# Kernel optimization log

Measured on AMD Instinct MI355X. Metric: run time of the kernel, lower is better.

Reference implementation:

```python
import jax, jax.numpy as jnp
import numpy as np

EPS = 1e-6


def setup_inputs() -> dict:
    key = jax.random.key(0)
    k1, k2 = jax.random.split(key)
    S, B, H, F = 4096, 8, 1024, 1024
    x = jax.random.normal(k1, (S, B, H), dtype=jnp.float32)
    scale = jnp.ones((H,), dtype=jnp.float32)
    ln_bias = jnp.zeros((H,), dtype=jnp.float32)
    # variance_scaling(1.0, 'fan_in', 'truncated_normal') ~ normal with std 1/sqrt(fan_in)
    kernel = jax.random.normal(k2, (H, F), dtype=jnp.float32) * (1.0 / np.sqrt(H))
    return {"x": x, "scale": scale, "ln_bias": ln_bias, "kernel": kernel}


def reference(x, scale, ln_bias, kernel):
    # LayerNorm over last (hidden) axis; zero_centered_gamma=False:
    #   y = (x - mean) / sqrt(var + eps) * gamma + beta
    mu = jnp.mean(x, axis=-1, keepdims=True)
    var = jnp.mean(jnp.square(x - mu), axis=-1, keepdims=True)
    ln_out = (x - mu) * jax.lax.rsqrt(var + EPS) * scale + ln_bias
    # DenseGeneral: contract hidden axis with kernel (H, F); use_bias=False, no depth scaling
    out = jnp.einsum("sbh,hf->sbf", ln_out, kernel)
    # return_layernorm_output=True -> (out, ln_out)
    return (out, ln_out)
```

## Files before the change

### kernel.cpp

```cpp
#include <hip/hip_runtime.h>
#include <stdint.h>

typedef unsigned short u16;

#define S_ 4096
#define B_ 8
#define H_ 1024
#define F_ 1024
#define M_ (S_ * B_)
#define N_ F_
#define K_ H_

#define BM 256
#define BN 256
#define BK 64
#define NT (K_ / BK)

typedef short short8 __attribute__((ext_vector_type(8)));
typedef float floatx4 __attribute__((ext_vector_type(4)));

__device__ __forceinline__ u16 f2bf(float f) {
    union { float f; uint32_t u; } c;
    c.f = f;
    uint32_t u = c.u;
    uint32_t r = (u + 0x7fffu + ((u >> 16) & 1u)) >> 16;
    return (u16)r;
}

__device__ __forceinline__ void async_load16(const void* gptr, void* lptr) {
    __builtin_amdgcn_global_load_lds(
        (const __attribute__((address_space(1))) uint32_t*)gptr,
        (__attribute__((address_space(3))) uint32_t*)lptr,
        16 , 0 , 0 );
}

__global__ __launch_bounds__(256) void transpose_cast_kernel(
    const float* __restrict__ w, u16* __restrict__ bt)
{
    __shared__ float tile[32][33];
    const int tx = threadIdx.x;
    const int ty = threadIdx.y;
    const int n0 = blockIdx.x * 32;
    const int k0 = blockIdx.y * 32;
#pragma unroll
    for (int j = 0; j < 4; ++j)
        tile[ty + j * 8][tx] = w[(size_t)(k0 + ty + j * 8) * N_ + n0 + tx];
    __syncthreads();
#pragma unroll
    for (int j = 0; j < 4; ++j)
        bt[(size_t)(n0 + ty + j * 8) * K_ + k0 + tx] =
            f2bf(tile[tx][ty + j * 8]);
}

#define LN_BLOCKS 2048
__global__ __launch_bounds__(256) void ln_kernel(
    const float* __restrict__ x, const float* __restrict__ scale,
    const float* __restrict__ bias, float* __restrict__ ln_out,
    u16* __restrict__ ln_bf16)
{
    const int lane = threadIdx.x & 63;
    const int wid  = (blockIdx.x << 2) | (threadIdx.x >> 6);
    const int nwaves = LN_BLOCKS * 4;

    float4 sc[4], bi[4];
#pragma unroll
    for (int j = 0; j < 4; ++j) {
        sc[j] = reinterpret_cast<const float4*>(scale)[j * 64 + lane];
        bi[j] = reinterpret_cast<const float4*>(bias)[j * 64 + lane];
    }

    for (int row = wid; row < M_; row += nwaves) {
        const float4* xr = reinterpret_cast<const float4*>(x + (size_t)row * H_);
        float4 v[4];
        float s = 0.f, sq = 0.f;
#pragma unroll
        for (int j = 0; j < 4; ++j) {
            v[j] = xr[j * 64 + lane];
            s  += v[j].x + v[j].y + v[j].z + v[j].w;
            sq += v[j].x * v[j].x + v[j].y * v[j].y +
                  v[j].z * v[j].z + v[j].w * v[j].w;
        }
#pragma unroll
        for (int off = 32; off >= 1; off >>= 1) {
            s  += __shfl_xor(s, off, 64);
            sq += __shfl_xor(sq, off, 64);
        }
        const float mu   = s * (1.0f / H_);
        const float var  = sq * (1.0f / H_) - mu * mu;
        const float rstd = rsqrtf(var + 1e-6f);

        float4* yr = reinterpret_cast<float4*>(ln_out + (size_t)row * H_);
        ushort4* hr = reinterpret_cast<ushort4*>(ln_bf16 + (size_t)row * H_);
#pragma unroll
        for (int j = 0; j < 4; ++j) {
            float4 y;
            y.x = (v[j].x - mu) * rstd * sc[j].x + bi[j].x;
            y.y = (v[j].y - mu) * rstd * sc[j].y + bi[j].y;
            y.z = (v[j].z - mu) * rstd * sc[j].z + bi[j].z;
            y.w = (v[j].w - mu) * rstd * sc[j].w + bi[j].w;
            yr[j * 64 + lane] = y;
            ushort4 h;
            h.x = f2bf(y.x); h.y = f2bf(y.y); h.z = f2bf(y.z); h.w = f2bf(y.w);
            hr[j * 64 + lane] = h;
        }
    }
}

__global__ __launch_bounds__(512, 2) void gemm_bt_kernel(
    const u16* __restrict__ A, const u16* __restrict__ Bt,
    float* __restrict__ C)
{
    __shared__ __align__(16) u16 As[2][BM * BK];
    __shared__ __align__(16) u16 Bs[2][BN * BK];

    const int tid  = threadIdx.x;
    const int wid  = tid >> 6;
    const int lane = tid & 63;
    const int wm   = wid >> 2;
    const int wn   = wid & 3;

    const int bid  = blockIdx.x;
    const int bx   = (bid >> 3) & 3;
    const int by   = ((bid >> 5) << 3) | (bid & 7);
    const int row0 = by * BM;
    const int col0 = bx * BN;

    floatx4 acc[8][4];
#pragma unroll
    for (int i = 0; i < 8; ++i)
#pragma unroll
        for (int j = 0; j < 4; ++j) acc[i][j] = (floatx4)0.0f;

    const int srow   = (wid << 3) | (lane >> 3);
    const int schunk = (lane & 7) ^ (srow & 7);
    const u16* Ag = A  + (size_t)(row0 + srow) * K_ + schunk * 8;
    const u16* Bg = Bt + (size_t)(col0 + srow) * K_ + schunk * 8;

#define STAGE(buf, kt) do {                                                   \
    const size_t koff_ = (size_t)(kt) * BK;                                   \
    _Pragma("unroll")                                                         \
    for (int i_ = 0; i_ < 4; ++i_) {                                          \
        async_load16(Ag + (size_t)(i_ * 64) * K_ + koff_,                     \
                     (char*)As[buf] + (size_t)(i_ * 64 + (wid << 3)) * 128);  \
        async_load16(Bg + (size_t)(i_ * 64) * K_ + koff_,                     \
                     (char*)Bs[buf] + (size_t)(i_ * 64 + (wid << 3)) * 128);  \
    }                                                                         \
} while (0)

    STAGE(0, 0);
    STAGE(1, 1);
    asm volatile("s_waitcnt vmcnt(8)" ::: "memory");
    __builtin_amdgcn_s_barrier();

    int cur = 0;
    for (int t = 0; t < NT; ++t) {
        short8 bfrag[4][2];
#pragma unroll
        for (int nt = 0; nt < 4; ++nt)
#pragma unroll
            for (int ks = 0; ks < 2; ++ks) {
                const int r  = (wn << 6) | (nt << 4) | (lane & 15);
                const int q  = (ks << 2) | (lane >> 4);
                const int cc = q ^ (r & 7);
                bfrag[nt][ks] = *reinterpret_cast<const short8*>(
                    (const char*)Bs[cur] + (size_t)r * 128 + cc * 16);
            }
#pragma unroll
        for (int mp = 0; mp < 4; ++mp) {
            short8 afrag[2][2];
#pragma unroll
            for (int mi = 0; mi < 2; ++mi)
#pragma unroll
                for (int ks = 0; ks < 2; ++ks) {
                    const int mt = mp * 2 + mi;
                    const int r  = (wm << 7) | (mt << 4) | (lane & 15);
                    const int q  = (ks << 2) | (lane >> 4);
                    const int cc = q ^ (r & 7);
                    afrag[mi][ks] = *reinterpret_cast<const short8*>(
                        (const char*)As[cur] + (size_t)r * 128 + cc * 16);
                }
            __builtin_amdgcn_s_setprio(1);
#pragma unroll
            for (int mi = 0; mi < 2; ++mi)
#pragma unroll
                for (int nt = 0; nt < 4; ++nt)
#pragma unroll
                    for (int ks = 0; ks < 2; ++ks)
                        acc[mp * 2 + mi][nt] =
                            __builtin_amdgcn_mfma_f32_16x16x32_bf16(
                                afrag[mi][ks], bfrag[nt][ks],
                                acc[mp * 2 + mi][nt], 0, 0, 0);
            __builtin_amdgcn_s_setprio(0);
        }

        if (t == NT - 1) break;
        asm volatile("s_waitcnt vmcnt(0) lgkmcnt(0)" ::: "memory");
        __builtin_amdgcn_s_barrier();
        if (t + 2 < NT) STAGE(cur, t + 2);
        cur ^= 1;
    }
#undef STAGE

#pragma unroll
    for (int mt = 0; mt < 8; ++mt) {
#pragma unroll
        for (int nt = 0; nt < 4; ++nt) {
            const int r0 = row0 + (wm << 7) + (mt << 4) + ((lane >> 4) << 2);
            const int c  = col0 + (wn << 6) + (nt << 4) + (lane & 15);
#pragma unroll
            for (int r = 0; r < 4; ++r)
                C[(size_t)(r0 + r) * N_ + c] = acc[mt][nt][r];
        }
    }
}

extern "C" void kernel_launch(void* const* d_in, const int* in_sizes, int n_in,
                              void* d_out, int out_size, void* d_ws, size_t ws_size,
                              hipStream_t stream) {
    const float* x      = (const float*)d_in[0];
    const float* scale  = (const float*)d_in[1];
    const float* lnbias = (const float*)d_in[2];
    const float* weight = (const float*)d_in[3];

    float* out    = (float*)d_out;
    float* ln_out = (float*)d_out + (size_t)M_ * N_;

    u16* ln_bf16 = (u16*)d_ws;
    u16* bt      = (u16*)d_ws + (size_t)M_ * K_;

    transpose_cast_kernel<<<dim3(N_ / 32, K_ / 32), dim3(32, 8), 0, stream>>>(
        weight, bt);
    ln_kernel<<<LN_BLOCKS, 256, 0, stream>>>(x, scale, lnbias, ln_out, ln_bf16);
    gemm_bt_kernel<<<(M_ / BM) * (N_ / BN), 512, 0, stream>>>(ln_bf16, bt, out);
}
```

Before: 451.5 us.

## Interleave staged async global-to-LDS loads with MFMA phases in GEMM loop

```diff
diff --git a/kernel.cpp b/kernel.cpp
--- a/kernel.cpp
+++ b/kernel.cpp
@@ -136,25 +136,57 @@
     const u16* Ag = A  + (size_t)(row0 + srow) * K_ + schunk * 8;
     const u16* Bg = Bt + (size_t)(col0 + srow) * K_ + schunk * 8;
 
-#define STAGE(buf, kt) do {                                                   \
-    const size_t koff_ = (size_t)(kt) * BK;                                   \
-    _Pragma("unroll")                                                         \
-    for (int i_ = 0; i_ < 4; ++i_) {                                          \
-        async_load16(Ag + (size_t)(i_ * 64) * K_ + koff_,                     \
-                     (char*)As[buf] + (size_t)(i_ * 64 + (wid << 3)) * 128);  \
-        async_load16(Bg + (size_t)(i_ * 64) * K_ + koff_,                     \
-                     (char*)Bs[buf] + (size_t)(i_ * 64 + (wid << 3)) * 128);  \
-    }                                                                         \
-} while (0)
-
-    STAGE(0, 0);
-    STAGE(1, 1);
-    asm volatile("s_waitcnt vmcnt(8)" ::: "memory");
-    __builtin_amdgcn_s_barrier();
-
-    int cur = 0;
+#define QSA(buf, kt, i)                                                       \
+    async_load16(Ag + (size_t)((i) * 64) * K_ + (size_t)(kt) * BK,            \
+                 (char*)As[buf] + (size_t)((i) * 64 + (wid << 3)) * 128)
+#define QSB(buf, kt, i)                                                       \
+    async_load16(Bg + (size_t)((i) * 64) * K_ + (size_t)(kt) * BK,            \
+                 (char*)Bs[buf] + (size_t)((i) * 64 + (wid << 3)) * 128)
+#define BARRIER() asm volatile("s_barrier" ::: "memory")
+
+#define LOADA(mp_)                                                            \
+    do {                                                                      \
+        _Pragma("unroll")                                                     \
+        for (int mi = 0; mi < 2; ++mi)                                        \
+            _Pragma("unroll")                                                 \
+            for (int ks = 0; ks < 2; ++ks) {                                  \
+                const int mt = (mp_) * 2 + mi;                                \
+                const int r  = (wm << 7) | (mt << 4) | (lane & 15);           \
+                const int q  = (ks << 2) | (lane >> 4);                       \
+                const int cc = q ^ (r & 7);                                   \
+                af[mi][ks] = *reinterpret_cast<const short8*>(                \
+                    (const char*)As[c] + (size_t)r * 128 + cc * 16);          \
+            }                                                                 \
+    } while (0)
+
+#define MFMA8(mp_)                                                            \
+    do {                                                                      \
+        __builtin_amdgcn_s_setprio(1);                                        \
+        _Pragma("unroll")                                                     \
+        for (int mi = 0; mi < 2; ++mi)                                        \
+            _Pragma("unroll")                                                 \
+            for (int nt = 0; nt < 4; ++nt)                                    \
+                _Pragma("unroll")                                             \
+                for (int ks = 0; ks < 2; ++ks)                                \
+                    acc[(mp_) * 2 + mi][nt] =                                 \
+                        __builtin_amdgcn_mfma_f32_16x16x32_bf16(              \
+                            af[mi][ks], bfrag[nt][ks],                        \
+                            acc[(mp_) * 2 + mi][nt], 0, 0, 0);                \
+        __builtin_amdgcn_s_setprio(0);                                        \
+    } while (0)
+
+#pragma unroll
+    for (int i = 0; i < 4; ++i) { QSA(0, 0, i); QSB(0, 0, i); }
+    QSA(1, 1, 0);
+    QSA(1, 1, 2);
+    asm volatile("s_waitcnt vmcnt(2)" ::: "memory");
+    BARRIER();
+
     for (int t = 0; t < NT; ++t) {
+        const int c = t & 1;
         short8 bfrag[4][2];
+        short8 af[2][2];
+
 #pragma unroll
         for (int nt = 0; nt < 4; ++nt)
 #pragma unroll
@@ -163,43 +195,43 @@
                 const int q  = (ks << 2) | (lane >> 4);
                 const int cc = q ^ (r & 7);
                 bfrag[nt][ks] = *reinterpret_cast<const short8*>(
-                    (const char*)Bs[cur] + (size_t)r * 128 + cc * 16);
+                    (const char*)Bs[c] + (size_t)r * 128 + cc * 16);
             }
-#pragma unroll
-        for (int mp = 0; mp < 4; ++mp) {
-            short8 afrag[2][2];
-#pragma unroll
-            for (int mi = 0; mi < 2; ++mi)
-#pragma unroll
-                for (int ks = 0; ks < 2; ++ks) {
-                    const int mt = mp * 2 + mi;
-                    const int r  = (wm << 7) | (mt << 4) | (lane & 15);
-                    const int q  = (ks << 2) | (lane >> 4);
-                    const int cc = q ^ (r & 7);
-                    afrag[mi][ks] = *reinterpret_cast<const short8*>(
-                        (const char*)As[cur] + (size_t)r * 128 + cc * 16);
-                }
-            __builtin_amdgcn_s_setprio(1);
-#pragma unroll
-            for (int mi = 0; mi < 2; ++mi)
-#pragma unroll
-                for (int nt = 0; nt < 4; ++nt)
-#pragma unroll
-                    for (int ks = 0; ks < 2; ++ks)
-                        acc[mp * 2 + mi][nt] =
-                            __builtin_amdgcn_mfma_f32_16x16x32_bf16(
-                                afrag[mi][ks], bfrag[nt][ks],
-                                acc[mp * 2 + mi][nt], 0, 0, 0);
-            __builtin_amdgcn_s_setprio(0);
-        }
-
-        if (t == NT - 1) break;
-        asm volatile("s_waitcnt vmcnt(0) lgkmcnt(0)" ::: "memory");
-        __builtin_amdgcn_s_barrier();
-        if (t + 2 < NT) STAGE(cur, t + 2);
-        cur ^= 1;
-    }
-#undef STAGE
+        LOADA(0);
+        if (t + 1 < NT) { QSA(c ^ 1, t + 1, 1); QSB(c ^ 1, t + 1, 0); }
+        BARRIER();
+        MFMA8(0);
+        BARRIER();
+
+        LOADA(1);
+        if (t + 1 < NT) { QSA(c ^ 1, t + 1, 3); QSB(c ^ 1, t + 1, 1); }
+        BARRIER();
+        MFMA8(1);
+        BARRIER();
+
+        LOADA(2);
+        if (t + 1 < NT) QSB(c ^ 1, t + 1, 2);
+        if (t + 2 < NT) QSA(c, t + 2, 0);
+        BARRIER();
+        MFMA8(2);
+        BARRIER();
+
+        LOADA(3);
+        if (t + 1 < NT) QSB(c ^ 1, t + 1, 3);
+        if (t + 2 < NT) QSA(c, t + 2, 2);
+        BARRIER();
+        MFMA8(3);
+        if (t + 1 < NT) {
+            if (t + 2 < NT) asm volatile("s_waitcnt vmcnt(1)" ::: "memory");
+            else            asm volatile("s_waitcnt vmcnt(0)" ::: "memory");
+            BARRIER();
+        }
+    }
+#undef QSA
+#undef QSB
+#undef BARRIER
+#undef LOADA
+#undef MFMA8
 
 #pragma unroll
     for (int mt = 0; mt < 8; ++mt) {
```

New measurement: 458.0 us. About the same (+1.4%).
